# Kernel tuning notes

Hardware: AMD Instinct MI355X
Metric: run time of the kernel (lower is better)

The kernel has to match this reference:

```python
import jax, jax.numpy as jnp
import numpy as np

VO, SO, VIN, SM = 16, 100, 16, 100
B, N, K = 2, 8192, 30
EPS = 1e-8

def _split(x, nv):
    v = x[..., :3 * nv].reshape(x.shape[:-1] + (nv, 3))
    s = x[..., 3 * nv:]
    return v, s

def _merge(v, s):
    return jnp.concatenate([v.reshape(v.shape[:-2] + (-1,)), s], axis=-1)

def _vnorm(v):  # [..., nv, 3] -> [..., nv]
    return jnp.sqrt(jnp.sum(v * v, axis=-1) + EPS)

def gvp(x, nv_in, Wh, Wv, Ws, bs, nls=True, nlv=True):
    v, s = _split(x, nv_in)
    vh = jnp.einsum('...ic,ih->...hc', v, Wh)          # vi -> h vector linear
    vn = _vnorm(vh)                                     # rotation-invariant norms
    s_out = jnp.concatenate([s, vn], axis=-1) @ Ws + bs
    if nls:
        s_out = jax.nn.relu(s_out)
    v_out = jnp.einsum('...hc,ho->...oc', vh, Wv)       # h -> vo vector linear
    if nlv:
        v_out = v_out * jax.nn.sigmoid(_vnorm(v_out))[..., None]
    return _merge(v_out, s_out)

def gvp_layernorm(x, nv, g, b):
    v, s = _split(x, nv)
    vn2 = jnp.sum(v * v, axis=-1, keepdims=True)        # [..., nv, 1]
    denom = jnp.sqrt(jnp.mean(vn2, axis=-2, keepdims=True) + EPS)
    v = v / denom
    mu = jnp.mean(s, axis=-1, keepdims=True)
    var = jnp.var(s, axis=-1, keepdims=True)
    s = (s - mu) / jnp.sqrt(var + 1e-5) * g + b
    return _merge(v, s)

def setup_inputs() -> dict:
    key = jax.random.key(0)
    ks = jax.random.split(key, 24)
    def W(i, shape):
        return jax.random.normal(ks[i], shape, dtype=jnp.float32) / np.float32(np.sqrt(shape[0]))
    d = {}
    d['h_V'] = jax.random.normal(ks[0], (B, N, 3 * VO + SO), dtype=jnp.float32)
    d['h_M'] = jax.random.normal(ks[1], (B, N, K, 3 * VIN + SM), dtype=jnp.float32)
    d['mask_V'] = jax.random.randint(ks[2], (B, N), 0, 2, dtype=jnp.int32)
    d['mask_attend'] = jax.random.randint(ks[3], (B, N, K), 0, 2, dtype=jnp.int32)
    # W_EV: GVP(vi=32,si=200,vo=16,so=100,h=32) -> GVP(16,100,16,100) -> GVP(16,100,16,100,no nl)
    d['Wh1'] = W(4, (32, 32)); d['Wv1'] = W(5, (32, 16)); d['Ws1'] = W(6, (232, 100)); d['bs1'] = jnp.zeros((100,), jnp.float32)
    d['Wh2'] = W(7, (16, 16)); d['Wv2'] = W(8, (16, 16)); d['Ws2'] = W(9, (116, 100)); d['bs2'] = jnp.zeros((100,), jnp.float32)
    d['Wh3'] = W(10, (16, 16)); d['Wv3'] = W(11, (16, 16)); d['Ws3'] = W(12, (116, 100)); d['bs3'] = jnp.zeros((100,), jnp.float32)
    # W_dh: GVP(vi=16,si=100,vo=32,so=400,h=32) -> GVP(vi=32,si=400,vo=16,so=100,h=32,no nl)
    d['Wh4'] = W(13, (16, 32)); d['Wv4'] = W(14, (32, 32)); d['Ws4'] = W(15, (132, 400)); d['bs4'] = jnp.zeros((400,), jnp.float32)
    d['Wh5'] = W(16, (32, 32)); d['Wv5'] = W(17, (32, 16)); d['Ws5'] = W(18, (432, 100)); d['bs5'] = jnp.zeros((100,), jnp.float32)
    d['ln0_g'] = jnp.ones((SO,), jnp.float32); d['ln0_b'] = jnp.zeros((SO,), jnp.float32)
    d['ln1_g'] = jnp.ones((SO,), jnp.float32); d['ln1_b'] = jnp.zeros((SO,), jnp.float32)
    return d

def reference(h_V, h_M, mask_V, mask_attend,
              Wh1, Wv1, Ws1, bs1, Wh2, Wv2, Ws2, bs2, Wh3, Wv3, Ws3, bs3,
              Wh4, Wv4, Ws4, bs4, Wh5, Wv5, Ws5, bs5,
              ln0_g, ln0_b, ln1_g, ln1_b):
    # expand node features over neighbor axis and vs_concat with messages
    hVe = jnp.broadcast_to(h_V[:, :, None, :], (B, N, K, h_V.shape[-1]))
    vV, sV = _split(hVe, VO)
    vM, sM = _split(h_M, VIN)
    h_EV = _merge(jnp.concatenate([vV, vM], axis=-2), jnp.concatenate([sV, sM], axis=-1))
    m = gvp(h_EV, VO + VIN, Wh1, Wv1, Ws1, bs1)
    m = gvp(m, VO, Wh2, Wv2, Ws2, bs2)
    m = gvp(m, VO, Wh3, Wv3, Ws3, bs3, nls=False, nlv=False)
    m = mask_attend[..., None].astype(jnp.float32) * m
    dh = jnp.mean(m, axis=2)
    h = gvp_layernorm(h_V + dh, VO, ln0_g, ln0_b)  # dropout rate 0 -> identity
    dh2 = gvp(h, VO, Wh4, Wv4, Ws4, bs4)
    dh2 = gvp(dh2, 2 * VO, Wh5, Wv5, Ws5, bs5, nls=False, nlv=False)
    h = gvp_layernorm(h + dh2, VO, ln1_g, ln1_b)
    h = mask_V[..., None].astype(jnp.float32) * h
    return h
```

## Files before the change

kernel.cpp:

```cpp
#include <hip/hip_runtime.h>

#define KK 30
#define F 148
#define NNODE 16384
#define NPB 16

typedef short bf16x8 __attribute__((ext_vector_type(8)));
typedef float f32x4v __attribute__((ext_vector_type(4)));

__device__ __forceinline__ ushort f2bf(float x) {
  unsigned u = __float_as_uint(x);
  unsigned r = (u + 0x7FFF + ((u >> 16) & 1)) >> 16;
  return (ushort)r;
}
__device__ __forceinline__ float bf2f(ushort b) { return __uint_as_float(((unsigned)b) << 16); }
__device__ __forceinline__ unsigned pk2(float x, float y) {
  return (unsigned)f2bf(x) | ((unsigned)f2bf(y) << 16);
}
__device__ __forceinline__ void bsplit(float x, ushort& h, ushort& l) {
  ushort hh = f2bf(x); h = hh; l = f2bf(x - bf2f(hh));
}

#define WS_S1B 0
#define WS_VHB (NNODE * 100)
#define WS_WSB (NNODE * 100 + NNODE * 96)
#define B1HI 0
#define B1LO 17920
#define B2HI 35840
#define B2LO 50176
#define B3HI 64512
#define B3LO 78848

__global__ void prep_weights(const float* __restrict__ Ws1, const float* __restrict__ Ws2,
                             const float* __restrict__ Ws3, ushort* __restrict__ ws) {
  int i = blockIdx.x * 256 + threadIdx.x;
  if (i < 17920) {
    int n = i / 160, k = i % 160;
    float w = (n < 100 && k < 132) ? Ws1[(100 + k) * 100 + n] : 0.f;
    ushort h, l; bsplit(w, h, l);
    ws[B1HI + i] = h; ws[B1LO + i] = l;
  } else if (i < 17920 + 14336) {
    int j = i - 17920; int n = j / 128, k = j % 128;
    float w = (n < 100 && k < 116) ? Ws2[k * 100 + n] : 0.f;
    ushort h, l; bsplit(w, h, l);
    ws[B2HI + j] = h; ws[B2LO + j] = l;
  } else if (i < 17920 + 2 * 14336) {
    int j = i - 17920 - 14336; int n = j / 128, k = j % 128;
    float w = (n < 100 && k < 116) ? Ws3[k * 100 + n] : 0.f;
    ushort h, l; bsplit(w, h, l);
    ws[B3HI + j] = h; ws[B3LO + j] = l;
  }
}

__global__ __launch_bounds__(256)
void prep_node(const float* __restrict__ h_V, const float* __restrict__ Ws1,
               const float* __restrict__ bs1, const float* __restrict__ Wh1,
               float* __restrict__ s1bg, float* __restrict__ vhbg) {
  __shared__ float wt[100 * 101];
  __shared__ float wh[512];
  __shared__ float svs[NPB * 148];
  const int tid = threadIdx.x;
  const long node0 = (long)blockIdx.x * NPB;
  for (int idx = tid; idx < 10000; idx += 256) {
    int i = idx / 100, n = idx - i * 100;
    wt[n * 101 + i] = Ws1[idx];
  }
  for (int idx = tid; idx < 512; idx += 256) wh[idx] = Wh1[idx];
  for (int idx = tid; idx < NPB * 148; idx += 256) {
    int nd = idx / 148, f = idx - nd * 148;
    svs[idx] = h_V[(node0 + nd) * 148 + f];
  }
  __syncthreads();
  for (int task = tid; task < NPB * 100; task += 256) {
    int nd = task / 100, n = task - nd * 100;
    const float* s = svs + nd * 148 + 48;
    const float* w = wt + n * 101;
    float acc = bs1[n];
#pragma unroll 10
    for (int i = 0; i < 100; i++) acc = fmaf(s[i], w[i], acc);
    s1bg[(node0 + nd) * 100 + n] = acc;
  }
  for (int task = tid; task < NPB * 32; task += 256) {
    int nd = task >> 5, h = task & 31;
    const float* s = svs + nd * 148;
    float a0 = 0.f, a1 = 0.f, a2 = 0.f;
#pragma unroll 4
    for (int i = 0; i < 16; i++) {
      float w = wh[i * 32 + h];
      a0 = fmaf(s[3*i], w, a0); a1 = fmaf(s[3*i+1], w, a1); a2 = fmaf(s[3*i+2], w, a2);
    }
    vhbg[(node0 + nd) * 96 + 3*h + 0] = a0;
    vhbg[(node0 + nd) * 96 + 3*h + 1] = a1;
    vhbg[(node0 + nd) * 96 + 3*h + 2] = a2;
  }
}

#define DECL12 float a00=0,a01=0,a02=0,a10=0,a11=0,a12=0,a20=0,a21=0,a22=0,a30=0,a31=0,a32=0;
#define FMA3x4(v0_,v1_,v2_,w_) \
  a00=fmaf(v0_,w_.x,a00); a01=fmaf(v1_,w_.x,a01); a02=fmaf(v2_,w_.x,a02); \
  a10=fmaf(v0_,w_.y,a10); a11=fmaf(v1_,w_.y,a11); a12=fmaf(v2_,w_.y,a12); \
  a20=fmaf(v0_,w_.z,a20); a21=fmaf(v1_,w_.z,a21); a22=fmaf(v2_,w_.z,a22); \
  a30=fmaf(v0_,w_.w,a30); a31=fmaf(v1_,w_.w,a31); a32=fmaf(v2_,w_.w,a32);

#define GATE3(x0,x1,x2,d0,d1,d2) { float vn_=sqrtf((x0)*(x0)+(x1)*(x1)+(x2)*(x2)+1e-8f); \
  float g_=1.f/(1.f+expf(-vn_)); d0=(x0)*g_; d1=(x1)*g_; d2=(x2)*g_; }

template<int NI, bool GATEF>
__device__ __forceinline__ void vtaskb(const unsigned* __restrict__ vsrc,
                                       const float* __restrict__ wbase, int wstride,
                                       float* __restrict__ vdst)
{
  DECL12
#pragma unroll 4
  for (int h2 = 0; h2 < NI / 2; h2++) {
    unsigned d0 = vsrc[3*h2+0], d1 = vsrc[3*h2+1], d2 = vsrc[3*h2+2];
    float4 w0 = *(const float4*)(wbase + (2*h2) * wstride);
    float4 w1 = *(const float4*)(wbase + (2*h2+1) * wstride);
    float e0 = bf2f((ushort)d0), e1 = bf2f((ushort)(d0 >> 16)), e2 = bf2f((ushort)d1);
    float g0 = bf2f((ushort)(d1 >> 16)), g1 = bf2f((ushort)d2), g2 = bf2f((ushort)(d2 >> 16));
    FMA3x4(e0, e1, e2, w0)
    FMA3x4(g0, g1, g2, w1)
  }
  if (GATEF) {
    GATE3(a00,a01,a02, vdst[0],vdst[1],vdst[2])
    GATE3(a10,a11,a12, vdst[3],vdst[4],vdst[5])
    GATE3(a20,a21,a22, vdst[6],vdst[7],vdst[8])
    GATE3(a30,a31,a32, vdst[9],vdst[10],vdst[11])
  } else {
    vdst[0]=a00; vdst[1]=a01; vdst[2]=a02;  vdst[3]=a10; vdst[4]=a11; vdst[5]=a12;
    vdst[6]=a20; vdst[7]=a21; vdst[8]=a22;  vdst[9]=a30; vdst[10]=a31; vdst[11]=a32;
  }
}

template<int NI>
__device__ __forceinline__ void v_vh_fused(const unsigned* vsrc,
                                           const float* __restrict__ Wv,
                                           const float* __restrict__ Whn,
                                           int c, int h0,
                                           unsigned* vrow_u, ushort* ncol)
{
  DECL12
#pragma unroll
  for (int h2 = 0; h2 < NI / 2; h2++) {
    unsigned d0 = vsrc[3*h2+0], d1 = vsrc[3*h2+1], d2 = vsrc[3*h2+2];
    float4 w0 = *(const float4*)(Wv + (2*h2) * 16);
    float4 w1 = *(const float4*)(Wv + (2*h2+1) * 16);
    float e0 = bf2f((ushort)d0), e1 = bf2f((ushort)(d0 >> 16)), e2 = bf2f((ushort)d1);
    float f0 = bf2f((ushort)(d1 >> 16)), f1 = bf2f((ushort)d2), f2 = bf2f((ushort)(d2 >> 16));
    FMA3x4(e0, e1, e2, w0)
    FMA3x4(f0, f1, f2, w1)
  }
  float g0,g1,g2,g3,g4,g5,g6,g7,g8,g9,g10,g11;
  GATE3(a00,a01,a02, g0,g1,g2)
  GATE3(a10,a11,a12, g3,g4,g5)
  GATE3(a20,a21,a22, g6,g7,g8)
  GATE3(a30,a31,a32, g9,g10,g11)
  a00=0;a01=0;a02=0;a10=0;a11=0;a12=0;a20=0;a21=0;a22=0;a30=0;a31=0;a32=0;
  {
    int ob = c * 4;
    float4 w;
    w = *(const float4*)(Whn + (ob+0)*16 + h0); FMA3x4(g0,g1,g2,w)
    w = *(const float4*)(Whn + (ob+1)*16 + h0); FMA3x4(g3,g4,g5,w)
    w = *(const float4*)(Whn + (ob+2)*16 + h0); FMA3x4(g6,g7,g8,w)
    w = *(const float4*)(Whn + (ob+3)*16 + h0); FMA3x4(g9,g10,g11,w)
  }
#define XCH_ACC(m_) { \
    float t0=__shfl_xor(g0,m_),  t1=__shfl_xor(g1,m_),  t2=__shfl_xor(g2,m_), \
          t3=__shfl_xor(g3,m_),  t4=__shfl_xor(g4,m_),  t5=__shfl_xor(g5,m_), \
          t6=__shfl_xor(g6,m_),  t7=__shfl_xor(g7,m_),  t8=__shfl_xor(g8,m_), \
          t9=__shfl_xor(g9,m_), t10=__shfl_xor(g10,m_), t11=__shfl_xor(g11,m_); \
    int ob = (c ^ m_) * 4; \
    float4 w; \
    w = *(const float4*)(Whn + (ob+0)*16 + h0); FMA3x4(t0,t1,t2,w) \
    w = *(const float4*)(Whn + (ob+1)*16 + h0); FMA3x4(t3,t4,t5,w) \
    w = *(const float4*)(Whn + (ob+2)*16 + h0); FMA3x4(t6,t7,t8,w) \
    w = *(const float4*)(Whn + (ob+3)*16 + h0); FMA3x4(t9,t10,t11,w) }
  XCH_ACC(1)
  XCH_ACC(2)
  XCH_ACC(3)
#undef XCH_ACC
  unsigned* vb = vrow_u + ((3 * h0) >> 1);
  vb[0]=pk2(a00,a01); vb[1]=pk2(a02,a10); vb[2]=pk2(a11,a12);
  vb[3]=pk2(a20,a21); vb[4]=pk2(a22,a30); vb[5]=pk2(a31,a32);
  float n0 = sqrtf(a00*a00+a01*a01+a02*a02 + 1e-8f);
  float n1 = sqrtf(a10*a10+a11*a11+a12*a12 + 1e-8f);
  float n2 = sqrtf(a20*a20+a21*a21+a22*a22 + 1e-8f);
  float n3 = sqrtf(a30*a30+a31*a31+a32*a32 + 1e-8f);
  unsigned* p = (unsigned*)ncol;
  p[0] = pk2(n0, n1); p[1] = pk2(n2, n3);
}

template<int NKS>
__device__ __forceinline__ void mfma_nt2(const ushort* __restrict__ A, int astr,
                                         const ushort* __restrict__ B_hi,
                                         const ushort* __restrict__ B_lo,
                                         int lane, f32x4v& c0, f32x4v& c1)
{
  int r = lane & 15, q = lane >> 4;
  const int ka = q * 8;
#pragma unroll
  for (int ks = 0; ks < NKS; ks++) {
    int ko = ka + ks * 32;
    bf16x8 a0 = *(const bf16x8*)(A + r * astr + ko);
    bf16x8 a1 = *(const bf16x8*)(A + (16 + r) * astr + ko);
    bf16x8 bh = *(const bf16x8*)(B_hi + ko);
    bf16x8 bl = *(const bf16x8*)(B_lo + ko);
    c0 = __builtin_amdgcn_mfma_f32_16x16x32_bf16(a0, bh, c0, 0, 0, 0);
    c0 = __builtin_amdgcn_mfma_f32_16x16x32_bf16(a0, bl, c0, 0, 0, 0);
    c1 = __builtin_amdgcn_mfma_f32_16x16x32_bf16(a1, bh, c1, 0, 0, 0);
    c1 = __builtin_amdgcn_mfma_f32_16x16x32_bf16(a1, bl, c1, 0, 0, 0);
  }
}

#define P_SV   0
#define P_MKB  148
#define P_DH   152
#define P_A2   252
#define P_A    2292
#define P_VA   4812
#define P_VB   6282
#define A1S 168
#define A2S 136
#define POOL_F 7722

__global__ __launch_bounds__(256, 5)
void mpnn_fused(const float* __restrict__ h_V, const float* __restrict__ h_M,
                const int* __restrict__ mask_V, const int* __restrict__ mask_attend,
                const float* __restrict__ Wh1, const float* __restrict__ Wv1,
                const float* __restrict__ Wv2, const float* __restrict__ bs2,
                const float* __restrict__ Wv3, const float* __restrict__ bs3,
                const float* __restrict__ Wh2, const float* __restrict__ Wh3,
                const float* __restrict__ Wh4, const float* __restrict__ Wv4,
                const float* __restrict__ Ws4, const float* __restrict__ bs4,
                const float* __restrict__ Wh5, const float* __restrict__ Wv5,
                const float* __restrict__ Ws5, const float* __restrict__ bs5,
                const float* __restrict__ ln0_g, const float* __restrict__ ln0_b,
                const float* __restrict__ ln1_g, const float* __restrict__ ln1_b,
                const float* __restrict__ s1bg, const float* __restrict__ vhbg,
                const ushort* __restrict__ wsb,
                float* __restrict__ out)
{
  __shared__ float pool[POOL_F];
  float* sv   = pool + P_SV;
  float* dhs  = pool + P_DH;
  float* VAp  = pool + P_VA;
  ushort* VBu = (ushort*)(pool + P_VB);
  ushort* A1 = (ushort*)(pool + P_A);
  ushort* A2 = (ushort*)(pool + P_A2);

  const int tid = threadIdx.x;
  const int node = blockIdx.x;
  const int wave = tid >> 6, lane = tid & 63;

  for (int f = tid; f < F; f += 256) sv[f] = h_V[(long)node * F + f];
  {
    unsigned long long bal = __ballot(tid < KK && mask_attend[node * KK + tid] != 0);
    if (tid == 0) *(unsigned*)(pool + P_MKB) = (unsigned)bal;
  }
  for (int t = tid; t < 420; t += 256) {
    int r = t / 14, c2 = t % 14;
    ((unsigned*)A1)[r * 84 + 66 + c2] = 0;
  }
  for (int t = tid; t < 180; t += 256) {
    int r = t / 6, c2 = t % 6;
    ((unsigned*)A2)[r * 68 + 58 + c2] = 0;
  }
  for (int task = tid; task < KK * 37; task += 256) {
    int k = task / 37, q = task % 37;
    float4 d = *(const float4*)(h_M + ((long)node * KK + k) * F + q * 4);
    if (q < 12) {
      VAp[k * 49 + q * 4 + 0] = d.x; VAp[k * 49 + q * 4 + 1] = d.y;
      VAp[k * 49 + q * 4 + 2] = d.z; VAp[k * 49 + q * 4 + 3] = d.w;
    } else {
      int j0 = q * 4 - 48;
      unsigned* p = (unsigned*)(A1 + k * A1S + j0);
      p[0] = (unsigned)f2bf(d.x) | ((unsigned)f2bf(d.y) << 16);
      p[1] = (unsigned)f2bf(d.z) | ((unsigned)f2bf(d.w) << 16);
    }
  }
  __syncthreads();

  if (tid < 240) {
    int k = tid >> 3, h0 = (tid & 7) * 4;
    const float4* vb4 = (const float4*)(vhbg + (long)node * 96 + 3 * h0);
    float4 q0 = vb4[0], q1 = vb4[1], q2 = vb4[2];
    float a00=q0.x,a01=q0.y,a02=q0.z, a10=q0.w,a11=q1.x,a12=q1.y,
          a20=q1.z,a21=q1.w,a22=q2.x, a30=q2.y,a31=q2.z,a32=q2.w;
#pragma unroll 4
    for (int i = 0; i < 16; i++) {
      float v0 = VAp[k*49+3*i], v1 = VAp[k*49+3*i+1], v2 = VAp[k*49+3*i+2];
      float4 w = *(const float4*)(Wh1 + (16 + i) * 32 + h0);
      FMA3x4(v0, v1, v2, w)
    }
    unsigned* vb = (unsigned*)(VBu + k * 96 + 3 * h0);
    vb[0]=pk2(a00,a01); vb[1]=pk2(a02,a10); vb[2]=pk2(a11,a12);
    vb[3]=pk2(a20,a21); vb[4]=pk2(a22,a30); vb[5]=pk2(a31,a32);
    float n0 = sqrtf(a00*a00+a01*a01+a02*a02 + 1e-8f);
    float n1 = sqrtf(a10*a10+a11*a11+a12*a12 + 1e-8f);
    float n2 = sqrtf(a20*a20+a21*a21+a22*a22 + 1e-8f);
    float n3 = sqrtf(a30*a30+a31*a31+a32*a32 + 1e-8f);
    unsigned* p = (unsigned*)(A1 + k * A1S + 100 + h0);
    p[0] = pk2(n0, n1); p[1] = pk2(n2, n3);
  }
  __syncthreads();

  if (wave < 2) {
    int r = lane & 15, q = lane >> 4;
    int nt0 = (wave == 0) ? 0 : 4, nt1 = (wave == 0) ? 4 : 7;
    for (int nt = nt0; nt < nt1; nt++) {
      int n = nt * 16 + r;
      float base = (n < 100) ? s1bg[(long)node * 100 + n] : 0.f;
      f32x4v c0 = {0,0,0,0}, c1 = {0,0,0,0};
      mfma_nt2<5>(A1, A1S, wsb + B1HI + n * 160, wsb + B1LO + n * 160, lane, c0, c1);
      unsigned* dst = (unsigned*)A2;
#pragma unroll
      for (int reg = 0; reg < 4; reg++) {
        int m0 = q * 4 + reg, m1 = m0 + 16;
        unsigned hx = f2bf(fmaxf(c0[reg] + base, 0.f));
        unsigned ox = __shfl_down(hx, 1);
        unsigned hy = f2bf(fmaxf(c1[reg] + base, 0.f));
        unsigned oy = __shfl_down(hy, 1);
        if (((lane & 1) == 0) && n < 100) {
          dst[(m0 * A2S + n) >> 1] = hx | (ox << 16);
          if (m1 < 30) dst[(m1 * A2S + n) >> 1] = hy | (oy << 16);
        }
      }
    }
  } else {
    int vt = tid - 128;
    if (vt < 120) {
      int k = vt >> 2, c = vt & 3, h0 = c * 4;
      v_vh_fused<32>((const unsigned*)(VBu + k * 96), Wv1 + h0, Wh2, c, h0,
                     (unsigned*)(VBu + k * 96), A2 + k * A2S + 100 + h0);
    }
  }
  __syncthreads();

  if (wave < 2) {
    int r = lane & 15, q = lane >> 4;
    int nt0 = (wave == 0) ? 0 : 4, nt1 = (wave == 0) ? 4 : 7;
    for (int nt = nt0; nt < nt1; nt++) {
      f32x4v c0 = {0,0,0,0}, c1 = {0,0,0,0};
      int n = nt * 16 + r;
      mfma_nt2<4>(A2, A2S, wsb + B2HI + n * 128, wsb + B2LO + n * 128, lane, c0, c1);
      float base = (n < 100) ? bs2[n] : 0.f;
      unsigned* dst = (unsigned*)A1;
#pragma unroll
      for (int reg = 0; reg < 4; reg++) {
        int m0 = q * 4 + reg, m1 = m0 + 16;
        unsigned hx = f2bf(fmaxf(c0[reg] + base, 0.f));
        unsigned ox = __shfl_down(hx, 1);
        unsigned hy = f2bf(fmaxf(c1[reg] + base, 0.f));
        unsigned oy = __shfl_down(hy, 1);
        if (((lane & 1) == 0) && n < 100) {
          dst[(m0 * A1S + n) >> 1] = hx | (ox << 16);
          if (m1 < 30) dst[(m1 * A1S + n) >> 1] = hy | (oy << 16);
        }
      }
    }
  } else {
    int vt = tid - 128;
    if (vt < 120) {
      int k = vt >> 2, c = vt & 3, h0 = c * 4;
      v_vh_fused<16>((const unsigned*)(VBu + k * 96), Wv2 + h0, Wh3, c, h0,
                     (unsigned*)(VBu + k * 96), A1 + k * A1S + 100 + h0);
    } else {
      for (int t = vt - 120; t < 180; t += 8) {
        int r = t / 6, c2 = t % 6;
        ((unsigned*)A1)[r * 84 + 58 + c2] = 0;
      }
    }
  }
  __syncthreads();

  if (wave < 2) {
    unsigned mkb = *(unsigned*)(pool + P_MKB);
    int r = lane & 15, q = lane >> 4;
    int nt0 = (wave == 0) ? 0 : 4, nt1 = (wave == 0) ? 4 : 7;
    for (int nt = nt0; nt < nt1; nt++) {
      f32x4v c0 = {0,0,0,0}, c1 = {0,0,0,0};
      int n = nt * 16 + r;
      mfma_nt2<4>(A1, A1S, wsb + B3HI + n * 128, wsb + B3LO + n * 128, lane, c0, c1);
      float part = 0.f;
#pragma unroll
      for (int reg = 0; reg < 4; reg++) {
        int m0 = q * 4 + reg, m1 = m0 + 16;
        part += ((mkb >> m0) & 1) ? c0[reg] : 0.f;
        part += ((mkb >> m1) & 1) ? c1[reg] : 0.f;
      }
      part += __shfl_xor(part, 16);
      part += __shfl_xor(part, 32);
      if (q == 0 && n < 100) dhs[n] = part;
    }
  } else {
    int vt = tid - 128;
    if (vt < 120) { int k = vt >> 2, o0 = (vt & 3) * 4;
      vtaskb<16, false>((const unsigned*)(VBu + k * 96), Wv3 + o0, 16, VAp + k*49 + 3*o0); }
  }
  __syncthreads();

  float* ns   = pool + P_A;
  float* xb   = ns;
  float* hb   = ns + 160;
  float* nvh4 = ns + 320;
  float* nvn4 = ns + 416;
  float* s4   = ns + 448;
  float* nvn5 = ns + 848;
  float* v4   = ns + 880;
  float* nvh5 = ns + 976;
  float* v5   = ns + 1072;
  float* s5   = ns + 1120;
  float* red  = ns + 1220;
  float* part = ns + 1232;

  {
    unsigned mkb = *(unsigned*)(pool + P_MKB);
    float cntf = (float)__popc(mkb);
    for (int f = tid; f < F; f += 256) {
      float acc;
      if (f < 48) { acc = 0.f; for (int k = 0; k < KK; k++) if ((mkb >> k) & 1) acc += VAp[k*49 + f]; }
      else        { int j = f - 48; acc = dhs[j] + cntf * bs3[j]; }
      xb[f] = sv[f] + acc * (1.f / (float)KK);
    }
  }
  __syncthreads();
  if (tid < 64) {
    float a = (tid < 50) ? xb[48 + 2 * tid] : 0.f;
    float b = (tid < 50) ? xb[48 + 2 * tid + 1] : 0.f;
    float s = a + b, qq = a * a + b * b;
    for (int off = 32; off; off >>= 1) { s += __shfl_down(s, off); qq += __shfl_down(qq, off); }
    if (tid == 0) { red[1] = s * 0.01f; red[2] = qq * 0.01f; }
  } else if (tid < 128) {
    int l = tid - 64;
    float v = (l < 48) ? xb[l] : 0.f;
    float qq = v * v;
    for (int off = 32; off; off >>= 1) qq += __shfl_down(qq, off);
    if (l == 0) red[0] = sqrtf(qq * (1.f / 16.f) + 1e-8f);
  }
  __syncthreads();
  {
    float denom = red[0], mu = red[1];
    float var = red[2] - mu * mu;
    float rs = rsqrtf(var + 1e-5f);
    for (int f = tid; f < F; f += 256) {
      if (f < 48) hb[f] = xb[f] / denom;
      else { int j = f - 48; hb[f] = (xb[f] - mu) * rs * ln0_g[j] + ln0_b[j]; }
    }
  }
  __syncthreads();

  if (tid < 32) {
    int h = tid;
    float a0 = 0.f, a1 = 0.f, a2 = 0.f;
#pragma unroll 4
    for (int i = 0; i < 16; i++) {
      float w = Wh4[i * 32 + h];
      a0 = fmaf(hb[3*i], w, a0); a1 = fmaf(hb[3*i+1], w, a1); a2 = fmaf(hb[3*i+2], w, a2);
    }
    nvh4[3*h] = a0; nvh4[3*h+1] = a1; nvh4[3*h+2] = a2;
    nvn4[h] = sqrtf(a0*a0 + a1*a1 + a2*a2 + 1e-8f);
  }
  __syncthreads();
  if (tid < 200) {
    int j0 = tid * 2;
    float ax = bs4[j0], ay = bs4[j0 + 1];
    const float* w = Ws4 + j0;
#pragma unroll 10
    for (int i = 0; i < 100; i++) {
      float s = hb[48 + i];
      float2 w2 = *(const float2*)(w + i * 400);
      ax = fmaf(s, w2.x, ax); ay = fmaf(s, w2.y, ay);
    }
#pragma unroll 8
    for (int h = 0; h < 32; h++) {
      float s = nvn4[h];
      float2 w2 = *(const float2*)(w + (100 + h) * 400);
      ax = fmaf(s, w2.x, ax); ay = fmaf(s, w2.y, ay);
    }
    s4[j0] = fmaxf(ax, 0.f); s4[j0 + 1] = fmaxf(ay, 0.f);
  } else if (tid >= 224) {
    int o = tid - 224;
    float a0 = 0.f, a1 = 0.f, a2 = 0.f;
#pragma unroll 4
    for (int h = 0; h < 32; h++) {
      float w = Wv4[h * 32 + o];
      a0 = fmaf(nvh4[3*h], w, a0); a1 = fmaf(nvh4[3*h+1], w, a1); a2 = fmaf(nvh4[3*h+2], w, a2);
    }
    GATE3(a0, a1, a2, v4[3*o], v4[3*o+1], v4[3*o+2])
  }
  __syncthreads();
  if (tid < 32) {
    int h = tid;
    float a0 = 0.f, a1 = 0.f, a2 = 0.f;
#pragma unroll 4
    for (int i = 0; i < 32; i++) {
      float w = Wh5[i * 32 + h];
      a0 = fmaf(v4[3*i], w, a0); a1 = fmaf(v4[3*i+1], w, a1); a2 = fmaf(v4[3*i+2], w, a2);
    }
    nvh5[3*h] = a0; nvh5[3*h+1] = a1; nvh5[3*h+2] = a2;
    nvn5[h] = sqrtf(a0*a0 + a1*a1 + a2*a2 + 1e-8f);
  }
  __syncthreads();
  if (tid < 200) {
    int jq = tid / 8, c = tid % 8, j0 = jq * 4;
    int ibeg = c * 54, iend = ibeg + 54;
    float4 acc = make_float4(0.f, 0.f, 0.f, 0.f);
    const float* w = Ws5 + j0;
#pragma unroll 6
    for (int i = ibeg; i < iend; i++) {
      float s = s4[i];
      float4 w4 = *(const float4*)(w + i * 100);
      acc.x = fmaf(s, w4.x, acc.x); acc.y = fmaf(s, w4.y, acc.y);
      acc.z = fmaf(s, w4.z, acc.z); acc.w = fmaf(s, w4.w, acc.w);
    }
    *(float4*)&part[tid * 4] = acc;
  } else if (tid >= 224 && tid < 240) {
    int o = tid - 224;
    float a0 = 0.f, a1 = 0.f, a2 = 0.f;
#pragma unroll 4
    for (int h = 0; h < 32; h++) {
      float w = Wv5[h * 16 + o];
      a0 = fmaf(nvh5[3*h], w, a0); a1 = fmaf(nvh5[3*h+1], w, a1); a2 = fmaf(nvh5[3*h+2], w, a2);
    }
    v5[3*o] = a0; v5[3*o+1] = a1; v5[3*o+2] = a2;
  }
  __syncthreads();
  if (tid < 25) {
    int j0 = tid * 4;
    float4 b = *(const float4*)(bs5 + j0);
    float4 acc = b;
#pragma unroll
    for (int c = 0; c < 8; c++) {
      float4 p = *(const float4*)&part[(tid * 8 + c) * 4];
      acc.x += p.x; acc.y += p.y; acc.z += p.z; acc.w += p.w;
    }
    *(float4*)&s5[j0] = acc;
  }
  __syncthreads();
  for (int f = tid; f < F; f += 256) {
    float d = (f < 48) ? v5[f] : s5[f - 48];
    xb[f] = hb[f] + d;
  }
  __syncthreads();
  if (tid < 64) {
    float a = (tid < 50) ? xb[48 + 2 * tid] : 0.f;
    float b = (tid < 50) ? xb[48 + 2 * tid + 1] : 0.f;
    float s = a + b, qq = a * a + b * b;
    for (int off = 32; off; off >>= 1) { s += __shfl_down(s, off); qq += __shfl_down(qq, off); }
    if (tid == 0) { red[1] = s * 0.01f; red[2] = qq * 0.01f; }
  } else if (tid < 128) {
    int l = tid - 64;
    float v = (l < 48) ? xb[l] : 0.f;
    float qq = v * v;
    for (int off = 32; off; off >>= 1) qq += __shfl_down(qq, off);
    if (l == 0) red[0] = sqrtf(qq * (1.f / 16.f) + 1e-8f);
  }
  __syncthreads();
  {
    float denom = red[0], mu = red[1];
    float var = red[2] - mu * mu;
    float rs = rsqrtf(var + 1e-5f);
    float mv = (float)mask_V[node];
    for (int f = tid; f < F; f += 256) {
      float val;
      if (f < 48) val = xb[f] / denom;
      else { int j = f - 48; val = (xb[f] - mu) * rs * ln1_g[j] + ln1_b[j]; }
      out[(long)node * F + f] = mv * val;
    }
  }
}

extern "C" void kernel_launch(void* const* d_in, const int* in_sizes, int n_in,
                              void* d_out, int out_size, void* d_ws, size_t ws_size,
                              hipStream_t stream) {
  const float* h_V  = (const float*)d_in[0];
  const float* h_M  = (const float*)d_in[1];
  const int* mask_V = (const int*)d_in[2];
  const int* mask_attend = (const int*)d_in[3];
  const float* Wh1 = (const float*)d_in[4];
  const float* Wv1 = (const float*)d_in[5];
  const float* Ws1 = (const float*)d_in[6];
  const float* bs1 = (const float*)d_in[7];
  const float* Wh2 = (const float*)d_in[8];
  const float* Wv2 = (const float*)d_in[9];
  const float* Ws2 = (const float*)d_in[10];
  const float* bs2 = (const float*)d_in[11];
  const float* Wh3 = (const float*)d_in[12];
  const float* Wv3 = (const float*)d_in[13];
  const float* Ws3 = (const float*)d_in[14];
  const float* bs3 = (const float*)d_in[15];
  const float* Wh4 = (const float*)d_in[16];
  const float* Wv4 = (const float*)d_in[17];
  const float* Ws4 = (const float*)d_in[18];
  const float* bs4 = (const float*)d_in[19];
  const float* Wh5 = (const float*)d_in[20];
  const float* Wv5 = (const float*)d_in[21];
  const float* Ws5 = (const float*)d_in[22];
  const float* bs5 = (const float*)d_in[23];
  const float* ln0_g = (const float*)d_in[24];
  const float* ln0_b = (const float*)d_in[25];
  const float* ln1_g = (const float*)d_in[26];
  const float* ln1_b = (const float*)d_in[27];
  float* out = (float*)d_out;

  float* wsf = (float*)d_ws;
  float* s1bg = wsf + WS_S1B;
  float* vhbg = wsf + WS_VHB;
  ushort* wsb = (ushort*)(wsf + WS_WSB);

  prep_weights<<<dim3(182), dim3(256), 0, stream>>>(Ws1, Ws2, Ws3, wsb);
  prep_node<<<dim3(NNODE / NPB), dim3(256), 0, stream>>>(h_V, Ws1, bs1, Wh1, s1bg, vhbg);
  mpnn_fused<<<dim3(NNODE), dim3(256), 0, stream>>>(
      h_V, h_M, mask_V, mask_attend,
      Wh1, Wv1, Wv2, bs2, Wv3, bs3, Wh2, Wh3,
      Wh4, Wv4, Ws4, bs4, Wh5, Wv5, Ws5, bs5,
      ln0_g, ln0_b, ln1_g, ln1_b, s1bg, vhbg, wsb, out);
}
```

Before: 1.327 ms.

## Split node tail into batched kernel and rotate MFMA/vector wave roles per block

Moves the per-node GVP layers 4-5 and both layernorms out of the per-node edge kernel into a separate node_tail kernel that handles 8 nodes per block, with the intermediate written to the output buffer. This is meant to stop 256 threads from sitting mostly idle through the serial per-node tail and to amortise weight loads across nodes. It also uses a hash of the node index to swap which waves do MFMA work and which do vector work, to balance load across SIMDs. In exchange it adds a global round-trip and an extra launch, and node_tail reads and writes the same buffer.

```diff
diff --git a/kernel.cpp b/kernel.cpp
--- a/kernel.cpp
+++ b/kernel.cpp
@@ -4,6 +4,7 @@
 #define F 148
 #define NNODE 16384
 #define NPB 16
+#define NPB2 8
 
 typedef short bf16x8 __attribute__((ext_vector_type(8)));
 typedef float f32x4v __attribute__((ext_vector_type(4)));
@@ -224,21 +225,15 @@
 #define POOL_F 7722
 
 __global__ __launch_bounds__(256, 5)
-void mpnn_fused(const float* __restrict__ h_V, const float* __restrict__ h_M,
-                const int* __restrict__ mask_V, const int* __restrict__ mask_attend,
-                const float* __restrict__ Wh1, const float* __restrict__ Wv1,
-                const float* __restrict__ Wv2, const float* __restrict__ bs2,
-                const float* __restrict__ Wv3, const float* __restrict__ bs3,
-                const float* __restrict__ Wh2, const float* __restrict__ Wh3,
-                const float* __restrict__ Wh4, const float* __restrict__ Wv4,
-                const float* __restrict__ Ws4, const float* __restrict__ bs4,
-                const float* __restrict__ Wh5, const float* __restrict__ Wv5,
-                const float* __restrict__ Ws5, const float* __restrict__ bs5,
-                const float* __restrict__ ln0_g, const float* __restrict__ ln0_b,
-                const float* __restrict__ ln1_g, const float* __restrict__ ln1_b,
-                const float* __restrict__ s1bg, const float* __restrict__ vhbg,
-                const ushort* __restrict__ wsb,
-                float* __restrict__ out)
+void mpnn_edge(const float* __restrict__ h_V, const float* __restrict__ h_M,
+               const int* __restrict__ mask_attend,
+               const float* __restrict__ Wh1, const float* __restrict__ Wv1,
+               const float* __restrict__ Wv2, const float* __restrict__ bs2,
+               const float* __restrict__ Wv3, const float* __restrict__ bs3,
+               const float* __restrict__ Wh2, const float* __restrict__ Wh3,
+               const float* __restrict__ s1bg, const float* __restrict__ vhbg,
+               const ushort* __restrict__ wsb,
+               float* __restrict__ xg)
 {
   __shared__ float pool[POOL_F];
   float* sv   = pool + P_SV;
@@ -251,6 +246,7 @@
   const int tid = threadIdx.x;
   const int node = blockIdx.x;
   const int wave = tid >> 6, lane = tid & 63;
+  const int vwave = wave ^ (int)(((unsigned)node * 0x9E3779B1u >> 16) & 2u);
 
   for (int f = tid; f < F; f += 256) sv[f] = h_V[(long)node * F + f];
   {
@@ -304,9 +300,9 @@
   }
   __syncthreads();
 
-  if (wave < 2) {
+  if (vwave < 2) {
     int r = lane & 15, q = lane >> 4;
-    int nt0 = (wave == 0) ? 0 : 4, nt1 = (wave == 0) ? 4 : 7;
+    int nt0 = (vwave == 0) ? 0 : 4, nt1 = (vwave == 0) ? 4 : 7;
     for (int nt = nt0; nt < nt1; nt++) {
       int n = nt * 16 + r;
       float base = (n < 100) ? s1bg[(long)node * 100 + n] : 0.f;
@@ -327,7 +323,7 @@
       }
     }
   } else {
-    int vt = tid - 128;
+    int vt = ((vwave - 2) << 6) + lane;
     if (vt < 120) {
       int k = vt >> 2, c = vt & 3, h0 = c * 4;
       v_vh_fused<32>((const unsigned*)(VBu + k * 96), Wv1 + h0, Wh2, c, h0,
@@ -336,9 +332,9 @@
   }
   __syncthreads();
 
-  if (wave < 2) {
+  if (vwave < 2) {
     int r = lane & 15, q = lane >> 4;
-    int nt0 = (wave == 0) ? 0 : 4, nt1 = (wave == 0) ? 4 : 7;
+    int nt0 = (vwave == 0) ? 0 : 4, nt1 = (vwave == 0) ? 4 : 7;
     for (int nt = nt0; nt < nt1; nt++) {
       f32x4v c0 = {0,0,0,0}, c1 = {0,0,0,0};
       int n = nt * 16 + r;
@@ -359,7 +355,7 @@
       }
     }
   } else {
-    int vt = tid - 128;
+    int vt = ((vwave - 2) << 6) + lane;
     if (vt < 120) {
       int k = vt >> 2, c = vt & 3, h0 = c * 4;
       v_vh_fused<16>((const unsigned*)(VBu + k * 96), Wv2 + h0, Wh3, c, h0,
@@ -373,10 +369,10 @@
   }
   __syncthreads();
 
-  if (wave < 2) {
+  if (vwave < 2) {
     unsigned mkb = *(unsigned*)(pool + P_MKB);
     int r = lane & 15, q = lane >> 4;
-    int nt0 = (wave == 0) ? 0 : 4, nt1 = (wave == 0) ? 4 : 7;
+    int nt0 = (vwave == 0) ? 0 : 4, nt1 = (vwave == 0) ? 4 : 7;
     for (int nt = nt0; nt < nt1; nt++) {
       f32x4v c0 = {0,0,0,0}, c1 = {0,0,0,0};
       int n = nt * 16 + r;
@@ -393,25 +389,11 @@
       if (q == 0 && n < 100) dhs[n] = part;
     }
   } else {
-    int vt = tid - 128;
+    int vt = ((vwave - 2) << 6) + lane;
     if (vt < 120) { int k = vt >> 2, o0 = (vt & 3) * 4;
       vtaskb<16, false>((const unsigned*)(VBu + k * 96), Wv3 + o0, 16, VAp + k*49 + 3*o0); }
   }
   __syncthreads();
-
-  float* ns   = pool + P_A;
-  float* xb   = ns;
-  float* hb   = ns + 160;
-  float* nvh4 = ns + 320;
-  float* nvn4 = ns + 416;
-  float* s4   = ns + 448;
-  float* nvn5 = ns + 848;
-  float* v4   = ns + 880;
-  float* nvh5 = ns + 976;
-  float* v5   = ns + 1072;
-  float* s5   = ns + 1120;
-  float* red  = ns + 1220;
-  float* part = ns + 1232;
 
   {
     unsigned mkb = *(unsigned*)(pool + P_MKB);
@@ -420,153 +402,173 @@
       float acc;
       if (f < 48) { acc = 0.f; for (int k = 0; k < KK; k++) if ((mkb >> k) & 1) acc += VAp[k*49 + f]; }
       else        { int j = f - 48; acc = dhs[j] + cntf * bs3[j]; }
-      xb[f] = sv[f] + acc * (1.f / (float)KK);
-    }
-  }
-  __syncthreads();
-  if (tid < 64) {
-    float a = (tid < 50) ? xb[48 + 2 * tid] : 0.f;
-    float b = (tid < 50) ? xb[48 + 2 * tid + 1] : 0.f;
-    float s = a + b, qq = a * a + b * b;
-    for (int off = 32; off; off >>= 1) { s += __shfl_down(s, off); qq += __shfl_down(qq, off); }
-    if (tid == 0) { red[1] = s * 0.01f; red[2] = qq * 0.01f; }
-  } else if (tid < 128) {
-    int l = tid - 64;
-    float v = (l < 48) ? xb[l] : 0.f;
-    float qq = v * v;
-    for (int off = 32; off; off >>= 1) qq += __shfl_down(qq, off);
-    if (l == 0) red[0] = sqrtf(qq * (1.f / 16.f) + 1e-8f);
-  }
-  __syncthreads();
-  {
-    float denom = red[0], mu = red[1];
-    float var = red[2] - mu * mu;
-    float rs = rsqrtf(var + 1e-5f);
-    for (int f = tid; f < F; f += 256) {
-      if (f < 48) hb[f] = xb[f] / denom;
-      else { int j = f - 48; hb[f] = (xb[f] - mu) * rs * ln0_g[j] + ln0_b[j]; }
-    }
-  }
-  __syncthreads();
-
-  if (tid < 32) {
-    int h = tid;
+      xg[(long)node * F + f] = sv[f] + acc * (1.f / (float)KK);
+    }
+  }
+}
+
+__global__ __launch_bounds__(256, 4)
+void node_tail(const float* __restrict__ xg, const int* __restrict__ mask_V,
+               const float* __restrict__ Wh4, const float* __restrict__ Wv4,
+               const float* __restrict__ Ws4, const float* __restrict__ bs4,
+               const float* __restrict__ Wh5, const float* __restrict__ Wv5,
+               const float* __restrict__ Ws5, const float* __restrict__ bs5,
+               const float* __restrict__ ln0_g, const float* __restrict__ ln0_b,
+               const float* __restrict__ ln1_g, const float* __restrict__ ln1_b,
+               float* __restrict__ out)
+{
+  __shared__ float xbs[NPB2][148];
+  __shared__ float hb[NPB2][160];
+  __shared__ float nvh4[NPB2][96];
+  __shared__ float nvn4[NPB2][32];
+  __shared__ float s4s[NPB2][432];
+  __shared__ float v4s[NPB2][96];
+  __shared__ float nvh5[NPB2][96];
+  __shared__ float v5s[NPB2][48];
+  __shared__ float s5s[NPB2][100];
+  __shared__ float red[NPB2][4];
+  const int tid = threadIdx.x;
+  const long node0 = (long)blockIdx.x * NPB2;
+
+  for (int idx = tid; idx < NPB2 * 148; idx += 256) {
+    int nd = idx / 148, f = idx - nd * 148;
+    xbs[nd][f] = xg[(node0 + nd) * 148 + f];
+  }
+  __syncthreads();
+  {
+    int nd = tid >> 5, l = tid & 31;
+    float a = 0.f, qq = 0.f, vq = 0.f;
+    for (int j = l; j < 100; j += 32) { float x = xbs[nd][48 + j]; a += x; qq = fmaf(x, x, qq); }
+    for (int j = l; j < 48; j += 32)  { float x = xbs[nd][j]; vq = fmaf(x, x, vq); }
+#pragma unroll
+    for (int off = 16; off; off >>= 1) {
+      a += __shfl_xor(a, off); qq += __shfl_xor(qq, off); vq += __shfl_xor(vq, off);
+    }
+    if (l == 0) {
+      red[nd][0] = sqrtf(vq * (1.f / 16.f) + 1e-8f);
+      red[nd][1] = a * 0.01f; red[nd][2] = qq * 0.01f;
+    }
+  }
+  __syncthreads();
+  for (int idx = tid; idx < NPB2 * 148; idx += 256) {
+    int nd = idx / 148, f = idx - nd * 148;
+    float denom = red[nd][0], mu = red[nd][1];
+    float rs = rsqrtf(red[nd][2] - mu * mu + 1e-5f);
+    hb[nd][f] = (f < 48) ? xbs[nd][f] / denom
+                         : (xbs[nd][f] - mu) * rs * ln0_g[f - 48] + ln0_b[f - 48];
+  }
+  __syncthreads();
+  {
+    int nd = tid >> 5, h = tid & 31;
     float a0 = 0.f, a1 = 0.f, a2 = 0.f;
 #pragma unroll 4
     for (int i = 0; i < 16; i++) {
       float w = Wh4[i * 32 + h];
-      a0 = fmaf(hb[3*i], w, a0); a1 = fmaf(hb[3*i+1], w, a1); a2 = fmaf(hb[3*i+2], w, a2);
-    }
-    nvh4[3*h] = a0; nvh4[3*h+1] = a1; nvh4[3*h+2] = a2;
-    nvn4[h] = sqrtf(a0*a0 + a1*a1 + a2*a2 + 1e-8f);
-  }
-  __syncthreads();
-  if (tid < 200) {
-    int j0 = tid * 2;
-    float ax = bs4[j0], ay = bs4[j0 + 1];
+      a0 = fmaf(hb[nd][3*i], w, a0); a1 = fmaf(hb[nd][3*i+1], w, a1); a2 = fmaf(hb[nd][3*i+2], w, a2);
+    }
+    nvh4[nd][3*h] = a0; nvh4[nd][3*h+1] = a1; nvh4[nd][3*h+2] = a2;
+    nvn4[nd][h] = sqrtf(a0*a0 + a1*a1 + a2*a2 + 1e-8f);
+  }
+  __syncthreads();
+  for (int task = tid; task < NPB2 * 100; task += 256) {
+    int nd = task / 100, jq = task - nd * 100, j0 = jq * 4;
+    float4 acc = *(const float4*)(bs4 + j0);
     const float* w = Ws4 + j0;
 #pragma unroll 10
     for (int i = 0; i < 100; i++) {
-      float s = hb[48 + i];
-      float2 w2 = *(const float2*)(w + i * 400);
-      ax = fmaf(s, w2.x, ax); ay = fmaf(s, w2.y, ay);
+      float s = hb[nd][48 + i];
+      float4 w4 = *(const float4*)(w + i * 400);
+      acc.x = fmaf(s, w4.x, acc.x); acc.y = fmaf(s, w4.y, acc.y);
+      acc.z = fmaf(s, w4.z, acc.z); acc.w = fmaf(s, w4.w, acc.w);
     }
 #pragma unroll 8
     for (int h = 0; h < 32; h++) {
-      float s = nvn4[h];
-      float2 w2 = *(const float2*)(w + (100 + h) * 400);
-      ax = fmaf(s, w2.x, ax); ay = fmaf(s, w2.y, ay);
-    }
-    s4[j0] = fmaxf(ax, 0.f); s4[j0 + 1] = fmaxf(ay, 0.f);
-  } else if (tid >= 224) {
-    int o = tid - 224;
+      float s = nvn4[nd][h];
+      float4 w4 = *(const float4*)(w + (100 + h) * 400);
+      acc.x = fmaf(s, w4.x, acc.x); acc.y = fmaf(s, w4.y, acc.y);
+      acc.z = fmaf(s, w4.z, acc.z); acc.w = fmaf(s, w4.w, acc.w);
+    }
+    acc.x = fmaxf(acc.x, 0.f); acc.y = fmaxf(acc.y, 0.f);
+    acc.z = fmaxf(acc.z, 0.f); acc.w = fmaxf(acc.w, 0.f);
+    *(float4*)&s4s[nd][j0] = acc;
+  }
+  {
+    int nd = tid >> 5, o = tid & 31;
     float a0 = 0.f, a1 = 0.f, a2 = 0.f;
-#pragma unroll 4
+#pragma unroll 8
     for (int h = 0; h < 32; h++) {
       float w = Wv4[h * 32 + o];
-      a0 = fmaf(nvh4[3*h], w, a0); a1 = fmaf(nvh4[3*h+1], w, a1); a2 = fmaf(nvh4[3*h+2], w, a2);
-    }
-    GATE3(a0, a1, a2, v4[3*o], v4[3*o+1], v4[3*o+2])
-  }
-  __syncthreads();
-  if (tid < 32) {
-    int h = tid;
+      a0 = fmaf(nvh4[nd][3*h], w, a0); a1 = fmaf(nvh4[nd][3*h+1], w, a1); a2 = fmaf(nvh4[nd][3*h+2], w, a2);
+    }
+    GATE3(a0, a1, a2, v4s[nd][3*o], v4s[nd][3*o+1], v4s[nd][3*o+2])
+  }
+  __syncthreads();
+  {
+    int nd = tid >> 5, h = tid & 31;
     float a0 = 0.f, a1 = 0.f, a2 = 0.f;
-#pragma unroll 4
+#pragma unroll 8
     for (int i = 0; i < 32; i++) {
       float w = Wh5[i * 32 + h];
-      a0 = fmaf(v4[3*i], w, a0); a1 = fmaf(v4[3*i+1], w, a1); a2 = fmaf(v4[3*i+2], w, a2);
-    }
-    nvh5[3*h] = a0; nvh5[3*h+1] = a1; nvh5[3*h+2] = a2;
-    nvn5[h] = sqrtf(a0*a0 + a1*a1 + a2*a2 + 1e-8f);
-  }
-  __syncthreads();
-  if (tid < 200) {
-    int jq = tid / 8, c = tid % 8, j0 = jq * 4;
-    int ibeg = c * 54, iend = ibeg + 54;
-    float4 acc = make_float4(0.f, 0.f, 0.f, 0.f);
+      a0 = fmaf(v4s[nd][3*i], w, a0); a1 = fmaf(v4s[nd][3*i+1], w, a1); a2 = fmaf(v4s[nd][3*i+2], w, a2);
+    }
+    nvh5[nd][3*h] = a0; nvh5[nd][3*h+1] = a1; nvh5[nd][3*h+2] = a2;
+    s4s[nd][400 + h] = sqrtf(a0*a0 + a1*a1 + a2*a2 + 1e-8f);
+  }
+  __syncthreads();
+  if (tid < NPB2 * 25) {
+    int nd = tid / 25, jq = tid - nd * 25, j0 = jq * 4;
+    float4 acc = *(const float4*)(bs5 + j0);
     const float* w = Ws5 + j0;
-#pragma unroll 6
-    for (int i = ibeg; i < iend; i++) {
-      float s = s4[i];
+#pragma unroll 8
+    for (int i = 0; i < 432; i++) {
+      float s = s4s[nd][i];
       float4 w4 = *(const float4*)(w + i * 100);
       acc.x = fmaf(s, w4.x, acc.x); acc.y = fmaf(s, w4.y, acc.y);
       acc.z = fmaf(s, w4.z, acc.z); acc.w = fmaf(s, w4.w, acc.w);
     }
-    *(float4*)&part[tid * 4] = acc;
-  } else if (tid >= 224 && tid < 240) {
-    int o = tid - 224;
-    float a0 = 0.f, a1 = 0.f, a2 = 0.f;
-#pragma unroll 4
-    for (int h = 0; h < 32; h++) {
-      float w = Wv5[h * 16 + o];
-      a0 = fmaf(nvh5[3*h], w, a0); a1 = fmaf(nvh5[3*h+1], w, a1); a2 = fmaf(nvh5[3*h+2], w, a2);
-    }
-    v5[3*o] = a0; v5[3*o+1] = a1; v5[3*o+2] = a2;
-  }
-  __syncthreads();
-  if (tid < 25) {
-    int j0 = tid * 4;
-    float4 b = *(const float4*)(bs5 + j0);
-    float4 acc = b;
+    *(float4*)&s5s[nd][j0] = acc;
+  } else if (tid >= 224) {
+    for (int t = tid - 224; t < NPB2 * 16; t += 32) {
+      int nd = t >> 4, o = t & 15;
+      float a0 = 0.f, a1 = 0.f, a2 = 0.f;
+#pragma unroll 8
+      for (int h = 0; h < 32; h++) {
+        float w = Wv5[h * 16 + o];
+        a0 = fmaf(nvh5[nd][3*h], w, a0); a1 = fmaf(nvh5[nd][3*h+1], w, a1); a2 = fmaf(nvh5[nd][3*h+2], w, a2);
+      }
+      v5s[nd][3*o] = a0; v5s[nd][3*o+1] = a1; v5s[nd][3*o+2] = a2;
+    }
+  }
+  __syncthreads();
+  for (int idx = tid; idx < NPB2 * 148; idx += 256) {
+    int nd = idx / 148, f = idx - nd * 148;
+    float d = (f < 48) ? v5s[nd][f] : s5s[nd][f - 48];
+    xbs[nd][f] = hb[nd][f] + d;
+  }
+  __syncthreads();
+  {
+    int nd = tid >> 5, l = tid & 31;
+    float a = 0.f, qq = 0.f, vq = 0.f;
+    for (int j = l; j < 100; j += 32) { float x = xbs[nd][48 + j]; a += x; qq = fmaf(x, x, qq); }
+    for (int j = l; j < 48; j += 32)  { float x = xbs[nd][j]; vq = fmaf(x, x, vq); }
 #pragma unroll
-    for (int c = 0; c < 8; c++) {
-      float4 p = *(const float4*)&part[(tid * 8 + c) * 4];
-      acc.x += p.x; acc.y += p.y; acc.z += p.z; acc.w += p.w;
-    }
-    *(float4*)&s5[j0] = acc;
-  }
-  __syncthreads();
-  for (int f = tid; f < F; f += 256) {
-    float d = (f < 48) ? v5[f] : s5[f - 48];
-    xb[f] = hb[f] + d;
-  }
-  __syncthreads();
-  if (tid < 64) {
-    float a = (tid < 50) ? xb[48 + 2 * tid] : 0.f;
-    float b = (tid < 50) ? xb[48 + 2 * tid + 1] : 0.f;
-    float s = a + b, qq = a * a + b * b;
-    for (int off = 32; off; off >>= 1) { s += __shfl_down(s, off); qq += __shfl_down(qq, off); }
-    if (tid == 0) { red[1] = s * 0.01f; red[2] = qq * 0.01f; }
-  } else if (tid < 128) {
-    int l = tid - 64;
-    float v = (l < 48) ? xb[l] : 0.f;
-    float qq = v * v;
-    for (int off = 32; off; off >>= 1) qq += __shfl_down(qq, off);
-    if (l == 0) red[0] = sqrtf(qq * (1.f / 16.f) + 1e-8f);
-  }
-  __syncthreads();
-  {
-    float denom = red[0], mu = red[1];
-    float var = red[2] - mu * mu;
-    float rs = rsqrtf(var + 1e-5f);
-    float mv = (float)mask_V[node];
-    for (int f = tid; f < F; f += 256) {
-      float val;
-      if (f < 48) val = xb[f] / denom;
-      else { int j = f - 48; val = (xb[f] - mu) * rs * ln1_g[j] + ln1_b[j]; }
-      out[(long)node * F + f] = mv * val;
-    }
+    for (int off = 16; off; off >>= 1) {
+      a += __shfl_xor(a, off); qq += __shfl_xor(qq, off); vq += __shfl_xor(vq, off);
+    }
+    if (l == 0) {
+      red[nd][0] = sqrtf(vq * (1.f / 16.f) + 1e-8f);
+      red[nd][1] = a * 0.01f; red[nd][2] = qq * 0.01f;
+    }
+  }
+  __syncthreads();
+  for (int idx = tid; idx < NPB2 * 148; idx += 256) {
+    int nd = idx / 148, f = idx - nd * 148;
+    float denom = red[nd][0], mu = red[nd][1];
+    float rs = rsqrtf(red[nd][2] - mu * mu + 1e-5f);
+    float mv = (float)mask_V[node0 + nd];
+    float val = (f < 48) ? xbs[nd][f] / denom
+                         : (xbs[nd][f] - mu) * rs * ln1_g[f - 48] + ln1_b[f - 48];
+    out[(node0 + nd) * 148 + f] = mv * val;
   }
 }
 
@@ -610,9 +612,11 @@
 
   prep_weights<<<dim3(182), dim3(256), 0, stream>>>(Ws1, Ws2, Ws3, wsb);
   prep_node<<<dim3(NNODE / NPB), dim3(256), 0, stream>>>(h_V, Ws1, bs1, Wh1, s1bg, vhbg);
-  mpnn_fused<<<dim3(NNODE), dim3(256), 0, stream>>>(
-      h_V, h_M, mask_V, mask_attend,
+  mpnn_edge<<<dim3(NNODE), dim3(256), 0, stream>>>(
+      h_V, h_M, mask_attend,
       Wh1, Wv1, Wv2, bs2, Wv3, bs3, Wh2, Wh3,
-      Wh4, Wv4, Ws4, bs4, Wh5, Wv5, Ws5, bs5,
-      ln0_g, ln0_b, ln1_g, ln1_b, s1bg, vhbg, wsb, out);
-}
+      s1bg, vhbg, wsb, out);
+  node_tail<<<dim3(NNODE / NPB2), dim3(256), 0, stream>>>(
+      out, mask_V, Wh4, Wv4, Ws4, bs4, Wh5, Wv5, Ws5, bs5,
+      ln0_g, ln0_b, ln1_g, ln1_b, out);
+}
```

Result: faster. 1.119 ms (-15.7%).
